# Optimization experiments

Measured on AMD Instinct MI355X. Metric: run time of the kernel, lower is better.

The kernel has to match this reference:

```python
import jax, jax.numpy as jnp
import numpy as np

HEADS = 16
DIM_HEAD = 64
CHUNK = 64
EPS_LN = 1e-5
EPS_T5 = 1e-6


def _layernorm(x, g, b):
    mu = x.mean(-1, keepdims=True)
    var = x.var(-1, keepdims=True)
    return (x - mu) / jnp.sqrt(var + EPS_LN) * g + b


def _t5norm(x, w):
    # T5LayerNorm variant: divide by (||x|| * d^-0.5), i.e. RMS norm
    norm = jnp.linalg.norm(x, axis=-1, keepdims=True) * (x.shape[-1] ** -0.5)
    return x / jnp.maximum(norm, EPS_T5) * w


def _rotary(t, freqs):
    rot = freqs.shape[-1]
    t1, t2 = t[..., :rot], t[..., rot:]
    half = rot // 2
    a, b = t1[..., :half], t1[..., half:]
    rh = jnp.concatenate((-b, a), axis=-1)  # rotate_half
    t1 = t1 * jnp.cos(freqs) + rh * jnp.sin(freqs)
    return jnp.concatenate((t1, t2), axis=-1)


def _split_heads(t):
    B, N, _ = t.shape
    return t.reshape(B, N, HEADS, DIM_HEAD).transpose(0, 2, 1, 3)


def _merge_heads(t):
    B, H, N, D = t.shape
    return t.transpose(0, 2, 1, 3).reshape(B, N, H * D)


def _attend(q, k, v, causal=False):
    sim = jnp.einsum('bhid,bhjd->bhij', q, k)
    if causal:
        i, j = sim.shape[-2:]
        m = jnp.triu(jnp.ones((i, j), bool), j - i + 1)
        sim = jnp.where(m, jnp.finfo(sim.dtype).min, sim)
    attn = jax.nn.softmax(sim, axis=-1)
    return jnp.einsum('bhij,bhjd->bhid', attn, v)


def setup_inputs() -> dict:
    key = jax.random.key(0)
    ks = jax.random.split(key, 20)
    b, n, d = 4, 1024, 1024
    kc, r, rn = n // CHUNK, 2, 2 * CHUNK
    dff = 4 * d
    s = 0.02

    def W(i, *shape):
        return jax.random.normal(ks[i], shape, jnp.float32) * s

    return {
        'hidden_states': jax.random.normal(ks[0], (b, n, d), jnp.float32),
        'retrieval': jax.random.normal(ks[1], (b, kc, r, rn, d), jnp.float32),
        'q_pos_emb': jax.random.normal(ks[2], (1, 1, CHUNK, DIM_HEAD), jnp.float32),
        'k_pos_emb': jax.random.normal(ks[3], (1, 1, rn, DIM_HEAD), jnp.float32),
        'ln1_g': jnp.ones(d), 'ln1_b': jnp.zeros(d),
        'Wq_s': W(4, d, d), 'Wk_s': W(5, d, d), 'Wv_s': W(6, d, d),
        'Wo_s': W(7, d, d), 'bo_s': jnp.zeros(d),
        'ln2_g': jnp.ones(d), 'ln2_b': jnp.zeros(d),
        'Wq_c': W(8, d, d), 'Wk_c': W(9, d, d), 'Wv_c': W(10, d, d),
        'Wo_c': W(11, d, d), 'bo_c': jnp.zeros(d),
        'null_k': jax.random.normal(ks[12], (d,), jnp.float32),
        'null_v': jax.random.normal(ks[13], (d,), jnp.float32),
        'post_w': jnp.ones(d),
        'W1': W(14, d, dff), 'b1': jnp.zeros(dff),
        'W2': W(15, dff, d), 'b2': jnp.zeros(d),
    }


def reference(hidden_states, retrieval, q_pos_emb, k_pos_emb,
              ln1_g, ln1_b, Wq_s, Wk_s, Wv_s, Wo_s, bo_s,
              ln2_g, ln2_b, Wq_c, Wk_c, Wv_c, Wo_c, bo_c,
              null_k, null_v, post_w, W1, b1, W2, b2):
    b, n, d = hidden_states.shape
    scale = DIM_HEAD ** -0.5

    # --- causal self-attention (pre-LN) ---
    x = _layernorm(hidden_states, ln1_g, ln1_b)
    q = _split_heads(x @ Wq_s) * scale
    k = _split_heads(x @ Wk_s)
    v = _split_heads(x @ Wv_s)
    o = _merge_heads(_attend(q, k, v, causal=True)) @ Wo_s + bo_s
    hs = _layernorm(o + hidden_states, ln2_g, ln2_b)
    residual = hs  # residual taken after ln_2, before cross-attn (per source)

    # --- chunked cross-attention over retrieved neighbor chunks ---
    kc, r, rn = retrieval.shape[1:4]
    cp = CHUNK - 1  # causal padding
    seq_index = (n // CHUNK) * CHUNK
    # shift queries back by chunk_size-1 (causality), pad tail with zeros
    xq = jnp.pad(hs[:, cp:], ((0, 0), (0, cp), (0, 0)))[:, :seq_index]
    xq = xq.reshape(b * kc, CHUNK, d)
    ctx = retrieval.reshape(b * kc, r * rn, d)
    qpe = jnp.pad(q_pos_emb[:, :, cp:], ((0, 0), (0, 0), (0, cp), (0, 0)))
    kpe = jnp.tile(k_pos_emb, (1, 1, r, 1))  # 'b h n d -> b h (r n) d'
    q = _rotary(_split_heads(xq @ Wq_c) * scale, qpe)
    kk = _rotary(_split_heads(ctx @ Wk_c), kpe)
    vv = _split_heads(ctx @ Wv_c)
    nk = jnp.broadcast_to(null_k.reshape(1, HEADS, 1, DIM_HEAD), (b * kc, HEADS, 1, DIM_HEAD))
    nv = jnp.broadcast_to(null_v.reshape(1, HEADS, 1, DIM_HEAD), (b * kc, HEADS, 1, DIM_HEAD))
    kk = jnp.concatenate((nk, kk), axis=2)
    vv = jnp.concatenate((nv, vv), axis=2)
    cca = _merge_heads(_attend(q, kk, vv)) @ Wo_c + bo_c
    cca = cca.reshape(b, seq_index, d)
    # shift output forward by chunk_size-1, crop to n
    cca = jnp.pad(cca, ((0, 0), (cp, 0), (0, 0)))[:, :n]
    # PostNorm wrapper: T5 norm of (fn(x) + x)
    hs = _t5norm(cca + hs, post_w)

    # --- GPTNeo MLP (gelu-new / tanh approx) ---
    ff = jax.nn.gelu(hs @ W1 + b1, approximate=True) @ W2 + b2
    return residual + ff
```

## Files before the change

kernel.cpp:

```cpp
#include <hip/hip_runtime.h>
#include <hip/hip_bf16.h>
#include <math.h>

using u16 = unsigned short;

static constexpr int SEQ = 1024;
static constexpr int DM  = 1024;
static constexpr int DHD = 64;

typedef __bf16 bfv8 __attribute__((ext_vector_type(8)));
typedef float  f32x4 __attribute__((ext_vector_type(4)));

__device__ __forceinline__ float u2f(u16 u) {
  return __uint_as_float(((unsigned int)u) << 16);
}
__device__ __forceinline__ u16 f2b(float x) {
  __hip_bfloat16 h = __float2bfloat16(x);
  return *reinterpret_cast<u16*>(&h);
}
__device__ __forceinline__ void gload16(const u16* g, u16* l) {
  __builtin_amdgcn_global_load_lds(
      (const __attribute__((address_space(1))) unsigned int*)g,
      (__attribute__((address_space(3))) unsigned int*)l, 16, 0, 0);
}

template <int OT, bool HASBIAS, bool HASRES, bool DOGELU, bool ROT, int DBUF, int PART>
__global__ __launch_bounds__(256) void mgemm_k(
    const u16* __restrict__ A, const u16* __restrict__ Bt, void* __restrict__ C,
    int M, int K, int lda, int ldc, int coff, float alpha0, float alpha1, int acol,
    const float* __restrict__ bias, const float* __restrict__ res,
    const float* __restrict__ tab) {
  constexpr int NBUF = DBUF ? 2 : 1;
  __shared__ u16 As[NBUF][128 * 64];
  __shared__ u16 Bs[NBUF][128 * 64];
  const int tid = threadIdx.x;
  const int w = tid >> 6, lane = tid & 63;
  const int wr = w >> 1, wc = w & 1;
  const int koff = blockIdx.z * K;

  const int nwg = gridDim.x * gridDim.y;
  const int bid = blockIdx.y * gridDim.x + blockIdx.x;
  const int qq = nwg >> 3, r8 = nwg & 7;
  const int xcd = bid & 7, pos = bid >> 3;
  const int cbase = (xcd < r8) ? xcd * (qq + 1) : r8 * (qq + 1) + (xcd - r8) * qq;
  const int logical = cbase + pos;
  const int row0 = (logical / gridDim.x) << 7;
  const int col0 = (logical % gridDim.x) << 7;

  f32x4 acc[4][4] = {};

  auto STAGE = [&](int buf, int k0) {
#pragma unroll
    for (int i = 0; i < 4; ++i) {
      const int c = ((w << 2) + i) * 64 + lane;
      const int r = c >> 3;
      const int cbs = ((c & 7) ^ (r & 7)) << 3;
      const int r64 = r & 63;
      const int rB = (r & 64) | ((r64 & 15) << 2) | (r64 >> 4);
      gload16(A + (size_t)(row0 + r) * lda + koff + k0 + cbs, &As[buf][((w << 2) + i) << 9]);
      gload16(Bt + (size_t)(col0 + rB) * lda + koff + k0 + cbs, &Bs[buf][((w << 2) + i) << 9]);
    }
  };
  auto COMPUTE = [&](int buf) {
#pragma unroll
    for (int kk = 0; kk < 2; ++kk) {
      bfv8 af[4], bfr[4];
#pragma unroll
      for (int m = 0; m < 4; ++m) {
        const int ar = (wr << 6) + (m << 4) + (lane & 15);
        const int sl = ((kk << 2) | (lane >> 4)) ^ (ar & 7);
        af[m] = *reinterpret_cast<const bfv8*>(&As[buf][ar * 64 + (sl << 3)]);
      }
#pragma unroll
      for (int n = 0; n < 4; ++n) {
        const int br = (wc << 6) + (n << 4) + (lane & 15);
        const int sl = ((kk << 2) | (lane >> 4)) ^ (br & 7);
        bfr[n] = *reinterpret_cast<const bfv8*>(&Bs[buf][br * 64 + (sl << 3)]);
      }
#pragma unroll
      for (int m = 0; m < 4; ++m)
#pragma unroll
        for (int n = 0; n < 4; ++n)
          acc[m][n] = __builtin_amdgcn_mfma_f32_16x16x32_bf16(af[m], bfr[n], acc[m][n], 0, 0, 0);
    }
  };

  if constexpr (DBUF) {
    STAGE(0, 0);
    int cur = 0;
    for (int k0 = 0; k0 < K; k0 += 64) {
      if (k0 + 64 < K) {
        STAGE(cur ^ 1, k0 + 64);
        asm volatile("s_waitcnt vmcnt(8)" ::: "memory");
      } else {
        asm volatile("s_waitcnt vmcnt(0)" ::: "memory");
      }
      __builtin_amdgcn_s_barrier();
      __builtin_amdgcn_sched_barrier(0);
      COMPUTE(cur);
      __builtin_amdgcn_s_barrier();
      cur ^= 1;
    }
  } else {
    for (int k0 = 0; k0 < K; k0 += 64) {
      STAGE(0, k0);
      __syncthreads();
      COMPUTE(0);
      __syncthreads();
    }
  }

  const int lr = (lane >> 4) << 2;
  const int lc = lane & 15;
  const int gcb = col0 + (wc << 6) + (lc << 2);
#pragma unroll
  for (int m = 0; m < 4; ++m) {
#pragma unroll
    for (int r = 0; r < 4; ++r) {
      const int gr = row0 + (wr << 6) + (m << 4) + lr + r;
      float t[4];
#pragma unroll
      for (int n = 0; n < 4; ++n)
        t[n] = acc[m][n][r] * ((gcb + n) < acol ? alpha0 : alpha1);
      if constexpr (ROT) {
        const int j = gr & 127;
        const int cc = gcb & 63;
        float4 c4 = *reinterpret_cast<const float4*>(tab + j * 64 + cc);
        float4 s4 = *reinterpret_cast<const float4*>(tab + 8192 + j * 64 + cc);
        const float cs[4] = {c4.x, c4.y, c4.z, c4.w};
        const float sn[4] = {s4.x, s4.y, s4.z, s4.w};
        float o2[4];
#pragma unroll
        for (int n = 0; n < 4; ++n) {
          const float pv = __shfl_xor(t[n], 8);
          const float part = (cc < 32) ? -pv : pv;
          o2[n] = t[n] * cs[n] + part * sn[n];
        }
#pragma unroll
        for (int n = 0; n < 4; ++n) t[n] = o2[n];
      }
      if constexpr (HASBIAS) {
        float4 b4 = *reinterpret_cast<const float4*>(bias + gcb);
        t[0] += b4.x; t[1] += b4.y; t[2] += b4.z; t[3] += b4.w;
      }
      if constexpr (DOGELU) {
#pragma unroll
        for (int n = 0; n < 4; ++n) {
          const float x = t[n];
          t[n] = 0.5f * x * (1.f + tanhf(0.7978845608f * (x + 0.044715f * x * x * x)));
        }
      }
      size_t cb = (size_t)gr * ldc + coff + gcb;
      if constexpr (PART) cb += (size_t)blockIdx.z * M * ldc;
      if constexpr (HASRES) {
        float4 r4 = *reinterpret_cast<const float4*>(res + cb);
        t[0] += r4.x; t[1] += r4.y; t[2] += r4.z; t[3] += r4.w;
      }
      if constexpr (OT == 0) {
        float4 o4 = make_float4(t[0], t[1], t[2], t[3]);
        *reinterpret_cast<float4*>((float*)C + cb) = o4;
      } else {
        ushort4 o4 = {f2b(t[0]), f2b(t[1]), f2b(t[2]), f2b(t[3])};
        *reinterpret_cast<ushort4*>((u16*)C + cb) = o4;
      }
    }
  }
}

__global__ __launch_bounds__(256) void reduce_k(const float* __restrict__ p,
                                                const float* __restrict__ bias,
                                                const float* __restrict__ res,
                                                float* __restrict__ out) {
  const int i = blockIdx.x * 256 + threadIdx.x;
  const int col = (i & 255) << 2;
  float4 a = reinterpret_cast<const float4*>(p)[i];
  float4 b = reinterpret_cast<const float4*>(p + (size_t)4096 * 1024)[i];
  float4 b4 = *reinterpret_cast<const float4*>(bias + col);
  float4 r4 = reinterpret_cast<const float4*>(res)[i];
  float4 o;
  o.x = a.x + b.x + b4.x + r4.x;
  o.y = a.y + b.y + b4.y + r4.y;
  o.z = a.z + b.z + b4.z + r4.z;
  o.w = a.w + b.w + b4.w + r4.w;
  reinterpret_cast<float4*>(out)[i] = o;
}

__global__ __launch_bounds__(256) void costab_k(const float* __restrict__ kpe,
                                                float* __restrict__ tab) {
  const int i = blockIdx.x * 256 + threadIdx.x;
  const float f = kpe[i];
  tab[i] = cosf(f);
  tab[8192 + i] = sinf(f);
}

struct WtArgs {
  const float* in[8];
  u16* out[8];
};
__global__ __launch_bounds__(256) void wtrans8_k(WtArgs a) {
  const float* in = a.in[blockIdx.z];
  u16* out = a.out[blockIdx.z];
  __shared__ float t[32][33];
  const int tx = threadIdx.x & 31, ty = threadIdx.x >> 5;
  const int r0 = blockIdx.y << 5, c0 = blockIdx.x << 5;
#pragma unroll
  for (int i = 0; i < 4; ++i)
    t[ty + 8 * i][tx] = in[(size_t)(r0 + ty + 8 * i) * 1024 + c0 + tx];
  __syncthreads();
#pragma unroll
  for (int i = 0; i < 4; ++i)
    out[(size_t)(c0 + ty + 8 * i) * 1024 + r0 + tx] = f2b(t[tx][ty + 8 * i]);
}

__global__ __launch_bounds__(256) void wtrans_k(const float* __restrict__ in,
                                                u16* __restrict__ out, int K, int N) {
  __shared__ float t[32][33];
  const int tx = threadIdx.x & 31, ty = threadIdx.x >> 5;
  const int r0 = blockIdx.y << 5, c0 = blockIdx.x << 5;
#pragma unroll
  for (int i = 0; i < 4; ++i)
    t[ty + 8 * i][tx] = in[(size_t)(r0 + ty + 8 * i) * N + c0 + tx];
  __syncthreads();
#pragma unroll
  for (int i = 0; i < 4; ++i)
    out[(size_t)(c0 + ty + 8 * i) * K + r0 + tx] = f2b(t[tx][ty + 8 * i]);
}

__global__ __launch_bounds__(256) void cast_k(const float* __restrict__ in,
                                              u16* __restrict__ out) {
  const int i = blockIdx.x * 256 + threadIdx.x;
  float4 v = reinterpret_cast<const float4*>(in)[i];
  ushort4 o = {f2b(v.x), f2b(v.y), f2b(v.z), f2b(v.w)};
  reinterpret_cast<ushort4*>(out)[i] = o;
}

__global__ __launch_bounds__(256) void ln_k(const float* __restrict__ in,
                                            const float* __restrict__ g,
                                            const float* __restrict__ b,
                                            u16* __restrict__ out) {
  const int tid = threadIdx.x;
  const int c = tid << 2;
  const size_t base = (size_t)blockIdx.x * DM;
  float4 x = *reinterpret_cast<const float4*>(in + base + c);
  float s = x.x + x.y + x.z + x.w;
  float ss = x.x * x.x + x.y * x.y + x.z * x.z + x.w * x.w;
#pragma unroll
  for (int m = 1; m < 64; m <<= 1) {
    s += __shfl_xor(s, m, 64);
    ss += __shfl_xor(ss, m, 64);
  }
  __shared__ float ls[4], lss[4];
  if ((tid & 63) == 0) { ls[tid >> 6] = s; lss[tid >> 6] = ss; }
  __syncthreads();
  s = (ls[0] + ls[1]) + (ls[2] + ls[3]);
  ss = (lss[0] + lss[1]) + (lss[2] + lss[3]);
  const float mu = s * (1.f / DM);
  const float var = ss * (1.f / DM) - mu * mu;
  const float rstd = rsqrtf(var + 1e-5f);
  float4 g4 = *reinterpret_cast<const float4*>(g + c);
  float4 b4 = *reinterpret_cast<const float4*>(b + c);
  ushort4 u;
  u.x = f2b((x.x - mu) * rstd * g4.x + b4.x);
  u.y = f2b((x.y - mu) * rstd * g4.y + b4.y);
  u.z = f2b((x.z - mu) * rstd * g4.z + b4.z);
  u.w = f2b((x.w - mu) * rstd * g4.w + b4.w);
  *reinterpret_cast<ushort4*>(out + base + c) = u;
}

__global__ __launch_bounds__(256) void ln2x_k(const float* __restrict__ in,
                                              const float* __restrict__ g,
                                              const float* __restrict__ b,
                                              float* __restrict__ hs,
                                              u16* __restrict__ xq) {
  const int tid = threadIdx.x;
  const int c = tid << 2;
  const int row = blockIdx.x;
  const size_t base = (size_t)row * DM;
  float4 x = *reinterpret_cast<const float4*>(in + base + c);
  float s = x.x + x.y + x.z + x.w;
  float ss = x.x * x.x + x.y * x.y + x.z * x.z + x.w * x.w;
#pragma unroll
  for (int m = 1; m < 64; m <<= 1) {
    s += __shfl_xor(s, m, 64);
    ss += __shfl_xor(ss, m, 64);
  }
  __shared__ float ls[4], lss[4];
  if ((tid & 63) == 0) { ls[tid >> 6] = s; lss[tid >> 6] = ss; }
  __syncthreads();
  s = (ls[0] + ls[1]) + (ls[2] + ls[3]);
  ss = (lss[0] + lss[1]) + (lss[2] + lss[3]);
  const float mu = s * (1.f / DM);
  const float var = ss * (1.f / DM) - mu * mu;
  const float rstd = rsqrtf(var + 1e-5f);
  float4 g4 = *reinterpret_cast<const float4*>(g + c);
  float4 b4 = *reinterpret_cast<const float4*>(b + c);
  float4 o;
  o.x = (x.x - mu) * rstd * g4.x + b4.x;
  o.y = (x.y - mu) * rstd * g4.y + b4.y;
  o.z = (x.z - mu) * rstd * g4.z + b4.z;
  o.w = (x.w - mu) * rstd * g4.w + b4.w;
  *reinterpret_cast<float4*>(hs + base + c) = o;
  const int local = row & (SEQ - 1);
  const int bb = row >> 10;
  if (local >= 63) {
    ushort4 u = {f2b(o.x), f2b(o.y), f2b(o.z), f2b(o.w)};
    *reinterpret_cast<ushort4*>(xq + (size_t)((bb << 10) + local - 63) * DM + c) = u;
  } else {
    ushort4 z = {0, 0, 0, 0};
    *reinterpret_cast<ushort4*>(xq + (size_t)((bb << 10) + 961 + local) * DM + c) = z;
  }
}

__global__ __launch_bounds__(256) void t5_k(const u16* __restrict__ cca,
                                            const float* __restrict__ hs,
                                            const float* __restrict__ w,
                                            u16* __restrict__ out) {
  const int tid = threadIdx.x;
  const int row = blockIdx.x;
  const int t = row & (SEQ - 1);
  const int c = tid << 2;
  const size_t base = (size_t)row * DM;
  float4 x = *reinterpret_cast<const float4*>(hs + base + c);
  if (t >= 63) {
    ushort4 cu = *reinterpret_cast<const ushort4*>(cca + base - (size_t)63 * DM + c);
    x.x += u2f(cu.x); x.y += u2f(cu.y); x.z += u2f(cu.z); x.w += u2f(cu.w);
  }
  float ss = x.x * x.x + x.y * x.y + x.z * x.z + x.w * x.w;
#pragma unroll
  for (int m = 1; m < 64; m <<= 1) ss += __shfl_xor(ss, m, 64);
  __shared__ float lss[4];
  if ((tid & 63) == 0) lss[tid >> 6] = ss;
  __syncthreads();
  ss = (lss[0] + lss[1]) + (lss[2] + lss[3]);
  const float rms = sqrtf(ss * (1.f / DM));
  const float inv = 1.f / fmaxf(rms, 1e-6f);
  float4 w4 = *reinterpret_cast<const float4*>(w + c);
  ushort4 o = {f2b(x.x * inv * w4.x), f2b(x.y * inv * w4.y),
               f2b(x.z * inv * w4.z), f2b(x.w * inv * w4.w)};
  *reinterpret_cast<ushort4*>(out + base + c) = o;
}

__global__ __launch_bounds__(256) void rotq_k(u16* __restrict__ q,
                                              const float* __restrict__ qpe) {
  __shared__ float rb[DM];
  const size_t base = (size_t)blockIdx.x * 64 * DM;
  const int e = threadIdx.x << 2;
  ushort4 u = *reinterpret_cast<const ushort4*>(q + base + e);
  rb[e + 0] = u2f(u.x); rb[e + 1] = u2f(u.y); rb[e + 2] = u2f(u.z); rb[e + 3] = u2f(u.w);
  __syncthreads();
  u16 ov[4];
#pragma unroll
  for (int k = 0; k < 4; ++k) {
    const int ee = e + k;
    const int cc = ee & 63;
    const float f = qpe[63 * 64 + cc];
    const float t1 = rb[ee];
    const float part = (cc < 32) ? -rb[ee + 32] : rb[ee - 32];
    ov[k] = f2b(t1 * cosf(f) + part * sinf(f));
  }
  ushort4 o = {ov[0], ov[1], ov[2], ov[3]};
  *reinterpret_cast<ushort4*>(q + base + e) = o;
}

__device__ __forceinline__ int vswz(int d, int k) {
  return (k & 7) | (((k >> 3) ^ ((d >> 2) & 7)) << 3);
}

__global__ __launch_bounds__(512) void attn_self_k(const u16* __restrict__ qkv,
                                                   u16* __restrict__ o) {
  const int qt = blockIdx.x, h = blockIdx.y, b = blockIdx.z;
  __shared__ u16 qs[128][72];
  __shared__ u16 ks[64][72];
  __shared__ u16 vt[64][72];
  __shared__ u16 ps[128][72];
  const int tid = threadIdx.x;
  const int w = tid >> 6, lane = tid & 63;
  const int strip = w << 4;
  const int sloc = (w & 3) << 4;
  const int lrow = lane & 15, lk = lane >> 4;
  const int rowb = b * SEQ;
  const int hoff = h * DHD;
  const int qrow0 = qt << 7;

#pragma unroll
  for (int rp = 0; rp < 4; ++rp) {
    const int fi = tid + (rp << 9);
    const int r = fi >> 4, c4 = (fi & 15) << 2;
    *reinterpret_cast<ushort4*>(&qs[r][c4]) =
        *reinterpret_cast<const ushort4*>(qkv + (size_t)(rowb + qrow0 + r) * 3072 + hoff + c4);
  }

  ushort4 kr[2], vr[2];
  auto loadKV = [&](int kt) {
#pragma unroll
    for (int rp = 0; rp < 2; ++rp) {
      const int fi = tid + (rp << 9);
      const int r = fi >> 4, c4 = (fi & 15) << 2;
      const size_t g = (size_t)(rowb + kt * 64 + r) * 3072 + hoff + c4;
      kr[rp] = *reinterpret_cast<const ushort4*>(qkv + g + 1024);
      vr[rp] = *reinterpret_cast<const ushort4*>(qkv + g + 2048);
    }
  };
  loadKV(0);

  const int ktmax = 2 * qt + 1;
  const int ktd = 2 * qt + (w >> 2);

  float mrun[4], lrun[4];
  f32x4 accO[4] = {};
#pragma unroll
  for (int r = 0; r < 4; ++r) { mrun[r] = -1e30f; lrun[r] = 0.f; }

  for (int kt = 0; kt <= ktmax; ++kt) {
    __syncthreads();
#pragma unroll
    for (int rp = 0; rp < 2; ++rp) {
      const int fi = tid + (rp << 9);
      const int r = fi >> 4, c4 = (fi & 15) << 2;
      *reinterpret_cast<ushort4*>(&ks[r][c4]) = kr[rp];
      vt[c4 + 0][vswz(c4 + 0, r)] = vr[rp].x;
      vt[c4 + 1][vswz(c4 + 1, r)] = vr[rp].y;
      vt[c4 + 2][vswz(c4 + 2, r)] = vr[rp].z;
      vt[c4 + 3][vswz(c4 + 3, r)] = vr[rp].w;
    }
    __syncthreads();
    if (kt < ktmax) loadKV(kt + 1);

    if (kt <= ktd) {
      f32x4 sacc[4] = {};
#pragma unroll
      for (int kk = 0; kk < 2; ++kk) {
        bfv8 qf = *reinterpret_cast<const bfv8*>(&qs[strip + lrow][(kk << 5) + (lk << 3)]);
#pragma unroll
        for (int n = 0; n < 4; ++n) {
          bfv8 kf = *reinterpret_cast<const bfv8*>(&ks[(n << 4) + lrow][(kk << 5) + (lk << 3)]);
          sacc[n] = __builtin_amdgcn_mfma_f32_16x16x32_bf16(qf, kf, sacc[n], 0, 0, 0);
        }
      }
      if (kt == ktd) {
#pragma unroll
        for (int n = 0; n < 4; ++n)
#pragma unroll
          for (int r = 0; r < 4; ++r)
            if ((n << 4) + lrow > sloc + (lk << 2) + r) sacc[n][r] = -1e30f;
      }
#pragma unroll
      for (int r = 0; r < 4; ++r) {
        float mt = fmaxf(fmaxf(sacc[0][r], sacc[1][r]), fmaxf(sacc[2][r], sacc[3][r]));
        mt = fmaxf(mt, __shfl_xor(mt, 1));
        mt = fmaxf(mt, __shfl_xor(mt, 2));
        mt = fmaxf(mt, __shfl_xor(mt, 4));
        mt = fmaxf(mt, __shfl_xor(mt, 8));
        const float nm = fmaxf(mrun[r], mt);
        const float f = __expf(mrun[r] - nm);
        mrun[r] = nm;
        float p0 = __expf(sacc[0][r] - nm);
        float p1 = __expf(sacc[1][r] - nm);
        float p2 = __expf(sacc[2][r] - nm);
        float p3 = __expf(sacc[3][r] - nm);
        float rs = (p0 + p1) + (p2 + p3);
        rs += __shfl_xor(rs, 1);
        rs += __shfl_xor(rs, 2);
        rs += __shfl_xor(rs, 4);
        rs += __shfl_xor(rs, 8);
        lrun[r] = lrun[r] * f + rs;
#pragma unroll
        for (int nd = 0; nd < 4; ++nd) accO[nd][r] *= f;
        const int prow = strip + (lk << 2) + r;
        ps[prow][lrow +  0] = f2b(p0);
        ps[prow][lrow + 16] = f2b(p1);
        ps[prow][lrow + 32] = f2b(p2);
        ps[prow][lrow + 48] = f2b(p3);
      }
#pragma unroll
      for (int kk = 0; kk < 2; ++kk) {
        bfv8 pf = *reinterpret_cast<const bfv8*>(&ps[strip + lrow][(kk << 5) + (lk << 3)]);
#pragma unroll
        for (int nd = 0; nd < 4; ++nd) {
          const int vd = (nd << 4) + lrow;
          const int slot = ((kk << 2) | lk) ^ ((vd >> 2) & 7);
          bfv8 vf = *reinterpret_cast<const bfv8*>(&vt[vd][slot << 3]);
          accO[nd] = __builtin_amdgcn_mfma_f32_16x16x32_bf16(pf, vf, accO[nd], 0, 0, 0);
        }
      }
    }
  }
#pragma unroll
  for (int r = 0; r < 4; ++r) {
    const float inv = 1.f / lrun[r];
    const size_t rowoff = (size_t)(rowb + qrow0 + strip + (lk << 2) + r) * DM + hoff;
#pragma unroll
    for (int nd = 0; nd < 4; ++nd)
      o[rowoff + (nd << 4) + lrow] = f2b(accO[nd][r] * inv);
  }
}

__global__ __launch_bounds__(256) void attn_cca_k(
    const u16* __restrict__ q, const u16* __restrict__ kv,
    const float* __restrict__ nullk, const float* __restrict__ nullv,
    u16* __restrict__ o) {
  const int h = blockIdx.y, bk = blockIdx.z;
  __shared__ u16 qs[64][72];
  __shared__ u16 ks[64][72];
  __shared__ u16 vt[64][72];
  __shared__ u16 ps[64][72];
  const int tid = threadIdx.x;
  const int w = tid >> 6, lane = tid & 63;
  const int strip = w << 4;
  const int lrow = lane & 15, lk = lane >> 4;
  const int hoff = h * DHD;
  const size_t qbase = (size_t)bk * 64 * DM + hoff;

#pragma unroll
  for (int rp = 0; rp < 4; ++rp) {
    const int fi = tid + (rp << 8);
    const int r = fi >> 4, c4 = (fi & 15) << 2;
    *reinterpret_cast<ushort4*>(&qs[r][c4]) =
        *reinterpret_cast<const ushort4*>(q + qbase + (size_t)r * DM + c4);
  }

  ushort4 kr[4], vr[4];
  auto loadKV = [&](int kt) {
#pragma unroll
    for (int rp = 0; rp < 4; ++rp) {
      const int fi = tid + (rp << 8);
      const int r = fi >> 4, c4 = (fi & 15) << 2;
      const int kj = kt * 64 + r;
      ushort4 ku = {0, 0, 0, 0}, vu = {0, 0, 0, 0};
      if (kj == 0) {
        float4 nk4 = *reinterpret_cast<const float4*>(nullk + hoff + c4);
        float4 nv4 = *reinterpret_cast<const float4*>(nullv + hoff + c4);
        ku = {f2b(nk4.x), f2b(nk4.y), f2b(nk4.z), f2b(nk4.w)};
        vu = {f2b(nv4.x), f2b(nv4.y), f2b(nv4.z), f2b(nv4.w)};
      } else if (kj <= 256) {
        const size_t g = (size_t)(bk * 256 + kj - 1) * 2048 + hoff + c4;
        ku = *reinterpret_cast<const ushort4*>(kv + g);
        vu = *reinterpret_cast<const ushort4*>(kv + g + 1024);
      }
      kr[rp] = ku; vr[rp] = vu;
    }
  };
  loadKV(0);

  float mrun[4], lrun[4];
  f32x4 accO[4] = {};
#pragma unroll
  for (int r = 0; r < 4; ++r) { mrun[r] = -1e30f; lrun[r] = 0.f; }

  for (int kt = 0; kt < 5; ++kt) {
    __syncthreads();
#pragma unroll
    for (int rp = 0; rp < 4; ++rp) {
      const int fi = tid + (rp << 8);
      const int r = fi >> 4, c4 = (fi & 15) << 2;
      *reinterpret_cast<ushort4*>(&ks[r][c4]) = kr[rp];
      vt[c4 + 0][vswz(c4 + 0, r)] = vr[rp].x;
      vt[c4 + 1][vswz(c4 + 1, r)] = vr[rp].y;
      vt[c4 + 2][vswz(c4 + 2, r)] = vr[rp].z;
      vt[c4 + 3][vswz(c4 + 3, r)] = vr[rp].w;
    }
    __syncthreads();
    if (kt < 4) loadKV(kt + 1);

    f32x4 sacc[4] = {};
#pragma unroll
    for (int kk = 0; kk < 2; ++kk) {
      bfv8 qf = *reinterpret_cast<const bfv8*>(&qs[strip + lrow][(kk << 5) + (lk << 3)]);
#pragma unroll
      for (int n = 0; n < 4; ++n) {
        bfv8 kf = *reinterpret_cast<const bfv8*>(&ks[(n << 4) + lrow][(kk << 5) + (lk << 3)]);
        sacc[n] = __builtin_amdgcn_mfma_f32_16x16x32_bf16(qf, kf, sacc[n], 0, 0, 0);
      }
    }
    if (kt == 4) {
#pragma unroll
      for (int n = 0; n < 4; ++n)
#pragma unroll
        for (int r = 0; r < 4; ++r)
          if ((n << 4) + lrow >= 1) sacc[n][r] = -1e30f;
    }
#pragma unroll
    for (int r = 0; r < 4; ++r) {
      float mt = fmaxf(fmaxf(sacc[0][r], sacc[1][r]), fmaxf(sacc[2][r], sacc[3][r]));
      mt = fmaxf(mt, __shfl_xor(mt, 1));
      mt = fmaxf(mt, __shfl_xor(mt, 2));
      mt = fmaxf(mt, __shfl_xor(mt, 4));
      mt = fmaxf(mt, __shfl_xor(mt, 8));
      const float nm = fmaxf(mrun[r], mt);
      const float f = __expf(mrun[r] - nm);
      mrun[r] = nm;
      float p0 = __expf(sacc[0][r] - nm);
      float p1 = __expf(sacc[1][r] - nm);
      float p2 = __expf(sacc[2][r] - nm);
      float p3 = __expf(sacc[3][r] - nm);
      float rs = (p0 + p1) + (p2 + p3);
      rs += __shfl_xor(rs, 1);
      rs += __shfl_xor(rs, 2);
      rs += __shfl_xor(rs, 4);
      rs += __shfl_xor(rs, 8);
      lrun[r] = lrun[r] * f + rs;
#pragma unroll
      for (int nd = 0; nd < 4; ++nd) accO[nd][r] *= f;
      const int prow = strip + (lk << 2) + r;
      ps[prow][lrow +  0] = f2b(p0);
      ps[prow][lrow + 16] = f2b(p1);
      ps[prow][lrow + 32] = f2b(p2);
      ps[prow][lrow + 48] = f2b(p3);
    }
#pragma unroll
    for (int kk = 0; kk < 2; ++kk) {
      bfv8 pf = *reinterpret_cast<const bfv8*>(&ps[strip + lrow][(kk << 5) + (lk << 3)]);
#pragma unroll
      for (int nd = 0; nd < 4; ++nd) {
        const int vd = (nd << 4) + lrow;
        const int slot = ((kk << 2) | lk) ^ ((vd >> 2) & 7);
        bfv8 vf = *reinterpret_cast<const bfv8*>(&vt[vd][slot << 3]);
        accO[nd] = __builtin_amdgcn_mfma_f32_16x16x32_bf16(pf, vf, accO[nd], 0, 0, 0);
      }
    }
  }
#pragma unroll
  for (int r = 0; r < 4; ++r) {
    const float inv = 1.f / lrun[r];
    const size_t rowoff = (size_t)(bk * 64 + strip + (lk << 2) + r) * DM + hoff;
#pragma unroll
    for (int nd = 0; nd < 4; ++nd)
      o[rowoff + (nd << 4) + lrow] = f2b(accO[nd][r] * inv);
  }
}

extern "C" void kernel_launch(void* const* d_in, const int* in_sizes, int n_in,
                              void* d_out, int out_size, void* d_ws, size_t ws_size,
                              hipStream_t stream) {
  const float* hidden    = (const float*)d_in[0];
  const float* retrieval = (const float*)d_in[1];
  const float* q_pos     = (const float*)d_in[2];
  const float* k_pos     = (const float*)d_in[3];
  const float* ln1_g     = (const float*)d_in[4];
  const float* ln1_b     = (const float*)d_in[5];
  const float* Wq_s      = (const float*)d_in[6];
  const float* Wk_s      = (const float*)d_in[7];
  const float* Wv_s      = (const float*)d_in[8];
  const float* Wo_s      = (const float*)d_in[9];
  const float* bo_s      = (const float*)d_in[10];
  const float* ln2_g     = (const float*)d_in[11];
  const float* ln2_b     = (const float*)d_in[12];
  const float* Wq_c      = (const float*)d_in[13];
  const float* Wk_c      = (const float*)d_in[14];
  const float* Wv_c      = (const float*)d_in[15];
  const float* Wo_c      = (const float*)d_in[16];
  const float* bo_c      = (const float*)d_in[17];
  const float* null_k    = (const float*)d_in[18];
  const float* null_v    = (const float*)d_in[19];
  const float* post_w    = (const float*)d_in[20];
  const float* W1        = (const float*)d_in[21];
  const float* b1        = (const float*)d_in[22];
  const float* W2        = (const float*)d_in[23];
  const float* b2        = (const float*)d_in[24];
  float* out = (float*)d_out;

  constexpr size_t MB = 1024 * 1024;
  constexpr size_t ME = 1024 * 1024;
  char* W = (char*)d_ws;
  u16* Wt_qkv  = (u16*)(W + 0 * MB);
  u16* Wt_os   = (u16*)(W + 6 * MB);
  u16* Wt_qc   = (u16*)(W + 8 * MB);
  u16* Wt_kcvc = (u16*)(W + 10 * MB);
  u16* Wt_oc   = (u16*)(W + 14 * MB);
  u16* W1t     = (u16*)(W + 16 * MB);
  u16* W2t     = (u16*)(W + 24 * MB);
  float* s5    = (float*)(W + 32 * MB);
  float* s0    = (float*)(W + 48 * MB);
  u16* retb    = (u16*)(W + 48 * MB);
  u16* ccab    = (u16*)(W + 48 * MB);
  u16* ccapb   = (u16*)(W + 56 * MB);
  u16* xb      = (u16*)(W + 64 * MB);
  u16* t5b     = (u16*)(W + 64 * MB);
  u16* attnb   = (u16*)(W + 80 * MB);
  u16* xqb     = (u16*)(W + 80 * MB);
  float* tab   = (float*)(W + 80 * MB);
  u16* qkvb    = (u16*)(W + 88 * MB);
  u16* qcb     = (u16*)(W + 88 * MB);
  u16* kkvvb   = (u16*)(W + 96 * MB);
  u16* ff1b    = (u16*)(W + 96 * MB);
  float* fpart = (float*)(W + 128 * MB);

  const dim3 blk(256);

  WtArgs wa;
  wa.in[0] = Wq_s; wa.out[0] = Wt_qkv + 0 * ME;
  wa.in[1] = Wk_s; wa.out[1] = Wt_qkv + 1 * ME;
  wa.in[2] = Wv_s; wa.out[2] = Wt_qkv + 2 * ME;
  wa.in[3] = Wo_s; wa.out[3] = Wt_os;
  wa.in[4] = Wq_c; wa.out[4] = Wt_qc;
  wa.in[5] = Wk_c; wa.out[5] = Wt_kcvc + 0 * ME;
  wa.in[6] = Wv_c; wa.out[6] = Wt_kcvc + 1 * ME;
  wa.in[7] = Wo_c; wa.out[7] = Wt_oc;
  wtrans8_k<<<dim3(32, 32, 8), blk, 0, stream>>>(wa);
  wtrans_k<<<dim3(128, 32), blk, 0, stream>>>(W1, W1t, 1024, 4096);
  wtrans_k<<<dim3(32, 128), blk, 0, stream>>>(W2, W2t, 4096, 1024);

  ln_k<<<dim3(4096), blk, 0, stream>>>(hidden, ln1_g, ln1_b, xb);
  mgemm_k<1, false, false, false, false, 1, 0><<<dim3(24, 32), blk, 0, stream>>>(
      xb, Wt_qkv, qkvb, 4096, 1024, 1024, 3072, 0, 0.125f, 1.f, 1024, nullptr, nullptr, nullptr);
  attn_self_k<<<dim3(8, 16, 4), dim3(512), 0, stream>>>(qkvb, attnb);
  mgemm_k<0, true, true, false, false, 1, 0><<<dim3(8, 32), blk, 0, stream>>>(
      attnb, Wt_os, s0, 4096, 1024, 1024, 1024, 0, 1.f, 1.f, 0, bo_s, hidden, nullptr);
  ln2x_k<<<dim3(4096), blk, 0, stream>>>(s0, ln2_g, ln2_b, s5, xqb);
  cast_k<<<dim3(16384), blk, 0, stream>>>(retrieval, retb);
  mgemm_k<1, false, false, false, false, 1, 0><<<dim3(8, 32), blk, 0, stream>>>(
      xqb, Wt_qc, qcb, 4096, 1024, 1024, 1024, 0, 1.f, 0.125f, 0, nullptr, nullptr, nullptr);
  rotq_k<<<dim3(64), blk, 0, stream>>>(qcb, q_pos);
  costab_k<<<dim3(32), blk, 0, stream>>>(k_pos, tab);
  mgemm_k<1, false, false, false, true, 1, 0><<<dim3(8, 128), blk, 0, stream>>>(
      retb, Wt_kcvc, kkvvb, 16384, 1024, 1024, 2048, 0, 1.f, 1.f, 0, nullptr, nullptr, tab);
  mgemm_k<1, false, false, false, false, 1, 0><<<dim3(8, 128), blk, 0, stream>>>(
      retb, Wt_kcvc + 1024 * 1024, kkvvb, 16384, 1024, 1024, 2048, 1024, 1.f, 1.f, 0,
      nullptr, nullptr, nullptr);
  attn_cca_k<<<dim3(1, 16, 64), blk, 0, stream>>>(qcb, kkvvb, null_k, null_v, ccab);
  mgemm_k<1, true, false, false, false, 1, 0><<<dim3(8, 32), blk, 0, stream>>>(
      ccab, Wt_oc, ccapb, 4096, 1024, 1024, 1024, 0, 1.f, 1.f, 0, bo_c, nullptr, nullptr);
  t5_k<<<dim3(4096), blk, 0, stream>>>(ccapb, s5, post_w, t5b);
  mgemm_k<1, true, false, true, false, 1, 0><<<dim3(32, 32), blk, 0, stream>>>(
      t5b, W1t, ff1b, 4096, 1024, 1024, 4096, 0, 1.f, 1.f, 0, b1, nullptr, nullptr);
  mgemm_k<0, false, false, false, false, 1, 1><<<dim3(8, 32, 2), blk, 0, stream>>>(
      ff1b, W2t, fpart, 4096, 2048, 4096, 1024, 0, 1.f, 1.f, 0, nullptr, nullptr, nullptr);
  reduce_k<<<dim3(4096), blk, 0, stream>>>(fpart, b2, s5, out);
}
```

Baseline: 444.2 us.

## Add 256x256-tile double-buffered GEMM kernel for the large projections

Adds a new 512-thread GEMM kernel that computes 256x256 output tiles with double-buffered LDS staging, swizzled shared-memory layout and XCD-aware block remapping. It replaces the 128-tile GEMM for the fused QKV projection, the two retrieval K/V projections (including the fused rotary epilogue) and the FF1 GELU GEMM. Larger tiles raise arithmetic intensity and cut global and LDS traffic per FLOP. The cost is 128 KB of LDS and heavy register use per block, which lowers occupancy, and fewer blocks per launch (192 to 256), which may leave CUs idle.

Result: faster. 425.6 us (-4.2%).

```diff
diff --git a/kernel.cpp b/kernel.cpp
--- a/kernel.cpp
+++ b/kernel.cpp
@@ -22,6 +22,137 @@
   __builtin_amdgcn_global_load_lds(
       (const __attribute__((address_space(1))) unsigned int*)g,
       (__attribute__((address_space(3))) unsigned int*)l, 16, 0, 0);
+}
+
+template <int OT, bool HASBIAS, bool DOGELU, bool ROT>
+__global__ __launch_bounds__(512) void mgemm256_k(
+    const u16* __restrict__ A, const u16* __restrict__ Bt, void* __restrict__ C,
+    int M, int K, int lda, int ldc, int coff, float alpha0, float alpha1, int acol,
+    const float* __restrict__ bias, const float* __restrict__ tab) {
+  __shared__ u16 As[2][256 * 64];
+  __shared__ u16 Bs[2][256 * 64];
+  const int tid = threadIdx.x;
+  const int w = tid >> 6, lane = tid & 63;
+  const int wm = w >> 2, wn = w & 3;
+  const int lc = lane & 15;
+
+  const int nwg = gridDim.x * gridDim.y;
+  const int bid = blockIdx.y * gridDim.x + blockIdx.x;
+  const int qq = nwg >> 3, r8 = nwg & 7;
+  const int xcd = bid & 7, pos = bid >> 3;
+  const int cbase = (xcd < r8) ? xcd * (qq + 1) : r8 * (qq + 1) + (xcd - r8) * qq;
+  const int logical = cbase + pos;
+  const int row0 = (logical / gridDim.x) << 8;
+  const int col0 = (logical % gridDim.x) << 8;
+
+  f32x4 acc[8][4] = {};
+
+  auto STAGE = [&](int buf, int k0) {
+#pragma unroll
+    for (int i = 0; i < 4; ++i) {
+      const int c = i * 512 + tid;
+      const int r = c >> 3;
+      const int cbs = ((c & 7) ^ (r & 7)) << 3;
+      gload16(A + (size_t)(row0 + r) * lda + k0 + cbs, &As[buf][c << 3]);
+    }
+#pragma unroll
+    for (int i = 0; i < 4; ++i) {
+      const int c = i * 512 + tid;
+      const int r = c >> 3;
+      const int cbs = ((c & 7) ^ (r & 7)) << 3;
+      const int r64 = r & 63;
+      const int rB = (r & 192) | ((r64 & 15) << 2) | (r64 >> 4);
+      gload16(Bt + (size_t)(col0 + rB) * lda + k0 + cbs, &Bs[buf][c << 3]);
+    }
+  };
+  auto COMPUTE = [&](int buf) {
+    bfv8 bc[2][4];
+#pragma unroll
+    for (int kk = 0; kk < 2; ++kk)
+#pragma unroll
+      for (int nr = 0; nr < 4; ++nr) {
+        const int br = (wn << 6) + (nr << 4) + lc;
+        const int sl = ((kk << 2) | (lane >> 4)) ^ (br & 7);
+        bc[kk][nr] = *reinterpret_cast<const bfv8*>(&Bs[buf][br * 64 + (sl << 3)]);
+      }
+#pragma unroll
+    for (int mr = 0; mr < 8; ++mr) {
+      const int ar = (wm << 7) + (mr << 4) + lc;
+      const int sl0 = (lane >> 4) ^ (ar & 7);
+      const int sl1 = (4 | (lane >> 4)) ^ (ar & 7);
+      bfv8 a0 = *reinterpret_cast<const bfv8*>(&As[buf][ar * 64 + (sl0 << 3)]);
+      bfv8 a1 = *reinterpret_cast<const bfv8*>(&As[buf][ar * 64 + (sl1 << 3)]);
+#pragma unroll
+      for (int nr = 0; nr < 4; ++nr) {
+        acc[mr][nr] = __builtin_amdgcn_mfma_f32_16x16x32_bf16(a0, bc[0][nr], acc[mr][nr], 0, 0, 0);
+        acc[mr][nr] = __builtin_amdgcn_mfma_f32_16x16x32_bf16(a1, bc[1][nr], acc[mr][nr], 0, 0, 0);
+      }
+    }
+  };
+
+  STAGE(0, 0);
+  int cur = 0;
+  for (int k0 = 0; k0 < K; k0 += 64) {
+    if (k0 + 64 < K) {
+      STAGE(cur ^ 1, k0 + 64);
+      asm volatile("s_waitcnt vmcnt(8)" ::: "memory");
+    } else {
+      asm volatile("s_waitcnt vmcnt(0)" ::: "memory");
+    }
+    __builtin_amdgcn_s_barrier();
+    __builtin_amdgcn_sched_barrier(0);
+    COMPUTE(cur);
+    __builtin_amdgcn_s_barrier();
+    cur ^= 1;
+  }
+
+  const int gcb = col0 + (wn << 6) + (lc << 2);
+#pragma unroll
+  for (int mr = 0; mr < 8; ++mr) {
+#pragma unroll
+    for (int r = 0; r < 4; ++r) {
+      const int gr = row0 + (wm << 7) + (mr << 4) + ((lane >> 4) << 2) + r;
+      float t[4];
+#pragma unroll
+      for (int nr = 0; nr < 4; ++nr)
+        t[nr] = acc[mr][nr][r] * ((gcb + nr) < acol ? alpha0 : alpha1);
+      if constexpr (ROT) {
+        const int j = gr & 127;
+        const int cc = gcb & 63;
+        float4 c4 = *reinterpret_cast<const float4*>(tab + j * 64 + cc);
+        float4 s4 = *reinterpret_cast<const float4*>(tab + 8192 + j * 64 + cc);
+        const float cs[4] = {c4.x, c4.y, c4.z, c4.w};
+        const float sn[4] = {s4.x, s4.y, s4.z, s4.w};
+        float o2[4];
+#pragma unroll
+        for (int nr = 0; nr < 4; ++nr) {
+          const float pv = __shfl_xor(t[nr], 8);
+          const float part = (cc < 32) ? -pv : pv;
+          o2[nr] = t[nr] * cs[nr] + part * sn[nr];
+        }
+#pragma unroll
+        for (int nr = 0; nr < 4; ++nr) t[nr] = o2[nr];
+      }
+      if constexpr (HASBIAS) {
+        float4 b4 = *reinterpret_cast<const float4*>(bias + gcb);
+        t[0] += b4.x; t[1] += b4.y; t[2] += b4.z; t[3] += b4.w;
+      }
+      if constexpr (DOGELU) {
+#pragma unroll
+        for (int nr = 0; nr < 4; ++nr) {
+          const float x = t[nr];
+          t[nr] = 0.5f * x * (1.f + tanhf(0.7978845608f * (x + 0.044715f * x * x * x)));
+        }
+      }
+      const size_t cb = (size_t)gr * ldc + coff + gcb;
+      if constexpr (OT == 0) {
+        *reinterpret_cast<float4*>((float*)C + cb) = make_float4(t[0], t[1], t[2], t[3]);
+      } else {
+        ushort4 o4 = {f2b(t[0]), f2b(t[1]), f2b(t[2]), f2b(t[3])};
+        *reinterpret_cast<ushort4*>((u16*)C + cb) = o4;
+      }
+    }
+  }
 }
 
 template <int OT, bool HASBIAS, bool HASRES, bool DOGELU, bool ROT, int DBUF, int PART>
@@ -701,8 +832,8 @@
   wtrans_k<<<dim3(32, 128), blk, 0, stream>>>(W2, W2t, 4096, 1024);
 
   ln_k<<<dim3(4096), blk, 0, stream>>>(hidden, ln1_g, ln1_b, xb);
-  mgemm_k<1, false, false, false, false, 1, 0><<<dim3(24, 32), blk, 0, stream>>>(
-      xb, Wt_qkv, qkvb, 4096, 1024, 1024, 3072, 0, 0.125f, 1.f, 1024, nullptr, nullptr, nullptr);
+  mgemm256_k<1, false, false, false><<<dim3(12, 16), dim3(512), 0, stream>>>(
+      xb, Wt_qkv, qkvb, 4096, 1024, 1024, 3072, 0, 0.125f, 1.f, 1024, nullptr, nullptr);
   attn_self_k<<<dim3(8, 16, 4), dim3(512), 0, stream>>>(qkvb, attnb);
   mgemm_k<0, true, true, false, false, 1, 0><<<dim3(8, 32), blk, 0, stream>>>(
       attnb, Wt_os, s0, 4096, 1024, 1024, 1024, 0, 1.f, 1.f, 0, bo_s, hidden, nullptr);
@@ -712,17 +843,17 @@
       xqb, Wt_qc, qcb, 4096, 1024, 1024, 1024, 0, 1.f, 0.125f, 0, nullptr, nullptr, nullptr);
   rotq_k<<<dim3(64), blk, 0, stream>>>(qcb, q_pos);
   costab_k<<<dim3(32), blk, 0, stream>>>(k_pos, tab);
-  mgemm_k<1, false, false, false, true, 1, 0><<<dim3(8, 128), blk, 0, stream>>>(
-      retb, Wt_kcvc, kkvvb, 16384, 1024, 1024, 2048, 0, 1.f, 1.f, 0, nullptr, nullptr, tab);
-  mgemm_k<1, false, false, false, false, 1, 0><<<dim3(8, 128), blk, 0, stream>>>(
+  mgemm256_k<1, false, false, true><<<dim3(4, 64), dim3(512), 0, stream>>>(
+      retb, Wt_kcvc, kkvvb, 16384, 1024, 1024, 2048, 0, 1.f, 1.f, 0, nullptr, tab);
+  mgemm256_k<1, false, false, false><<<dim3(4, 64), dim3(512), 0, stream>>>(
       retb, Wt_kcvc + 1024 * 1024, kkvvb, 16384, 1024, 1024, 2048, 1024, 1.f, 1.f, 0,
-      nullptr, nullptr, nullptr);
+      nullptr, nullptr);
   attn_cca_k<<<dim3(1, 16, 64), blk, 0, stream>>>(qcb, kkvvb, null_k, null_v, ccab);
   mgemm_k<1, true, false, false, false, 1, 0><<<dim3(8, 32), blk, 0, stream>>>(
       ccab, Wt_oc, ccapb, 4096, 1024, 1024, 1024, 0, 1.f, 1.f, 0, bo_c, nullptr, nullptr);
   t5_k<<<dim3(4096), blk, 0, stream>>>(ccapb, s5, post_w, t5b);
-  mgemm_k<1, true, false, true, false, 1, 0><<<dim3(32, 32), blk, 0, stream>>>(
-      t5b, W1t, ff1b, 4096, 1024, 1024, 4096, 0, 1.f, 1.f, 0, b1, nullptr, nullptr);
+  mgemm256_k<1, true, true, false><<<dim3(16, 16), dim3(512), 0, stream>>>(
+      t5b, W1t, ff1b, 4096, 1024, 1024, 4096, 0, 1.f, 1.f, 0, b1, nullptr);
   mgemm_k<0, false, false, false, false, 1, 1><<<dim3(8, 32, 2), blk, 0, stream>>>(
       ff1b, W2t, fpart, 4096, 2048, 4096, 1024, 0, 1.f, 1.f, 0, nullptr, nullptr, nullptr);
   reduce_k<<<dim3(4096), blk, 0, stream>>>(fpart, b2, s5, out);
```
